# Kernel tuning notes

Measured on AMD Instinct MI355X. Metric: run time of the kernel, lower is better.

Reference implementation:

```python
import jax, jax.numpy as jnp
import numpy as np

N = 100000   # nodes
E = 1600000  # edges
F_IN = 4
H = 64
G = 1000     # graphs in batch
C = 3        # num_classes
L = 2        # num_unit (LEConv layers)


def setup_inputs() -> dict:
    key = jax.random.key(0)
    ks = jax.random.split(key, 14)
    s = 0.1
    return {
        "x": jax.random.normal(ks[0], (N, F_IN), jnp.float32),
        "edge_index": jax.random.randint(ks[1], (2, E), 0, N, dtype=jnp.int32),
        "edge_attr": jax.random.uniform(ks[2], (E,), jnp.float32),
        "batch": jnp.sort(jax.random.randint(ks[3], (N,), 0, G, dtype=jnp.int32)),
        "w_emb": jax.random.normal(ks[4], (F_IN, H), jnp.float32) * s,
        "b_emb": jnp.zeros((H,), jnp.float32),
        "lin1_w": jax.random.normal(ks[5], (L, H, H), jnp.float32) * s,
        "lin1_b": jnp.zeros((L, H), jnp.float32),
        "lin2_w": jax.random.normal(ks[6], (L, H, H), jnp.float32) * s,  # bias=False in PyG LEConv
        "lin3_w": jax.random.normal(ks[7], (L, H, H), jnp.float32) * s,
        "lin3_b": jnp.zeros((L, H), jnp.float32),
        "mlp_w1": jax.random.normal(ks[8], (H, 2 * H), jnp.float32) * s,
        "mlp_b1": jnp.zeros((2 * H,), jnp.float32),
        "mlp_w2": jax.random.normal(ks[9], (2 * H, C), jnp.float32) * s,
        "mlp_b2": jnp.zeros((C,), jnp.float32),
    }


def reference(x, edge_index, edge_attr, batch, w_emb, b_emb,
              lin1_w, lin1_b, lin2_w, lin3_w, lin3_b,
              mlp_w1, mlp_b1, mlp_w2, mlp_b2):
    src, dst = edge_index[0], edge_index[1]  # message flows src(j) -> dst(i)
    h = x @ w_emb + b_emb  # [N, H]
    for l in range(L):
        a = h @ lin1_w[l] + lin1_b[l]            # lin1(x_j) source side
        b = h @ lin2_w[l]                         # lin2(x_i) target side, no bias
        msg = (a[src] - b[dst]) * edge_attr[:, None]   # [E, H]
        agg = jax.ops.segment_sum(msg, dst, num_segments=N)
        h = jax.nn.relu(agg + h @ lin3_w[l] + lin3_b[l])
    # global_mean_pool
    sums = jax.ops.segment_sum(h, batch, num_segments=G)        # [G, H]
    counts = jax.ops.segment_sum(jnp.ones((N,), h.dtype), batch, num_segments=G)
    graph_x = sums / jnp.maximum(counts, 1.0)[:, None]
    # causal_mlp head
    return jax.nn.relu(graph_x @ mlp_w1 + mlp_b1) @ mlp_w2 + mlp_b2  # [G, C]
```

## Files before the change

### kernel.cpp

```cpp
#include <hip/hip_runtime.h>

#define N_NODES 100000
#define N_EDGES 1600000
#define F_INPUT 4
#define HDIM 64
#define G_GRAPHS 1000
#define C_CLS 3

#define NPB 256
#define BSHIFT 8
#define NB 391
#define CBLK 98
#define CSR_CAP 6144
#define HIST_BLOCKS 512
#define BNDS_BLOCKS 391

typedef __attribute__((ext_vector_type(8))) short bf16x8;
typedef __attribute__((ext_vector_type(4))) float f32x4;

__device__ __forceinline__ unsigned short f2bf(float f) {
    unsigned u = __float_as_uint(f);
    unsigned r = (u + 0x7FFF + ((u >> 16) & 1)) >> 16;
    return (unsigned short)r;
}
__device__ __forceinline__ float bflo(unsigned u) {
    return __uint_as_float(u << 16);
}
__device__ __forceinline__ float bfhi(unsigned u) {
    return __uint_as_float(u & 0xFFFF0000u);
}
__device__ __forceinline__ float bf1(unsigned short s) {
    return __uint_as_float(((unsigned)s) << 16);
}

__global__ __launch_bounds__(256) void k_prew(
    const float* __restrict__ w_emb, const float* __restrict__ b_emb,
    const float* __restrict__ lin1_w, const float* __restrict__ lin1_b,
    const float* __restrict__ lin2_w,
    const float* __restrict__ lin3_w, const float* __restrict__ lin3_b,
    float* __restrict__ wp, float* __restrict__ bp, int* __restrict__ bcnt) {
    int t = threadIdx.x;
    for (int i = t; i < NB; i += 256) bcnt[i] = 0;
    int k = t >> 6, f = t & 63;
    const float* Ws[3] = {lin1_w, lin2_w, lin3_w};
#pragma unroll
    for (int m = 0; m < 3; ++m) {
        float s = 0.f;
        for (int j = 0; j < HDIM; ++j) s += w_emb[k * HDIM + j] * Ws[m][j * HDIM + f];
        wp[m * 256 + k * HDIM + f] = s;
    }
    if (t < HDIM) {
#pragma unroll
        for (int m = 0; m < 3; ++m) {
            float s = 0.f;
            for (int j = 0; j < HDIM; ++j) s += b_emb[j] * Ws[m][j * HDIM + t];
            if (m == 0) s += lin1_b[t];
            if (m == 2) s += lin3_b[t];
            bp[m * HDIM + t] = s;
        }
    }
}

__global__ __launch_bounds__(256) void k_hist_bounds(
    const int* __restrict__ dst, int* __restrict__ bcnt,
    const int* __restrict__ batch, int* __restrict__ goff) {
    __shared__ int s[NB];
    if (blockIdx.x < HIST_BLOCKS) {
        int bb = blockIdx.x;
        for (int i = threadIdx.x; i < NB; i += 256) s[i] = 0;
        __syncthreads();
        for (int e = bb * 256 + threadIdx.x; e < N_EDGES; e += HIST_BLOCKS * 256)
            atomicAdd(&s[dst[e] >> BSHIFT], 1);
        __syncthreads();
        for (int i = threadIdx.x; i < NB; i += 256)
            if (s[i]) atomicAdd(&bcnt[i], s[i]);
    } else {
        int n = (blockIdx.x - HIST_BLOCKS) * 256 + threadIdx.x;
        if (n >= N_NODES) return;
        int bv = batch[n];
        int bp_ = (n == 0) ? -1 : batch[n - 1];
        for (int g = bp_ + 1; g <= bv; ++g) goff[g] = n;
        if (n == N_NODES - 1) {
            for (int g = bv + 1; g <= G_GRAPHS; ++g) goff[g] = N_NODES;
        }
    }
}

__global__ __launch_bounds__(512) void k_boff(
    const int* __restrict__ bcnt, int* __restrict__ boff, int* __restrict__ bcur) {
    __shared__ int s[512];
    int t = threadIdx.x;
    int v = (t < NB) ? bcnt[t] : 0;
    s[t] = v;
    __syncthreads();
    for (int d = 1; d < 512; d <<= 1) {
        int x2 = (t >= d) ? s[t - d] : 0;
        __syncthreads();
        s[t] += x2;
        __syncthreads();
    }
    int ex = s[t] - v;
    if (t < NB) { boff[t] = ex; bcur[t] = ex; }
    if (t == 0) boff[NB] = N_EDGES;
}

__global__ __launch_bounds__(1024) void k_bucket(const int* __restrict__ src,
                                                 const int* __restrict__ dst,
                                                 const float* __restrict__ attr,
                                                 int* __restrict__ bcur,
                                                 int2* __restrict__ bbuf) {
    __shared__ int cnt[NB];
    __shared__ int base[NB];
    for (int i = threadIdx.x; i < NB; i += 1024) cnt[i] = 0;
    __syncthreads();
    int e0 = blockIdx.x * 16384;
    int myb[16], myrank[16];
    int2 mypack[16];
#pragma unroll
    for (int k = 0; k < 16; ++k) {
        int e = e0 + k * 1024 + threadIdx.x;
        if (e < N_EDGES) {
            int d = dst[e];
            int b = d >> BSHIFT;
            myb[k] = b;
            myrank[k] = atomicAdd(&cnt[b], 1);
            mypack[k].x = src[e] | ((d & (NPB - 1)) << 17);
            mypack[k].y = __float_as_int(attr[e]);
        } else
            myb[k] = -1;
    }
    __syncthreads();
    for (int i = threadIdx.x; i < NB; i += 1024)
        base[i] = cnt[i] ? atomicAdd(&bcur[i], cnt[i]) : 0;
    __syncthreads();
#pragma unroll
    for (int k = 0; k < 16; ++k)
        if (myb[k] >= 0) bbuf[base[myb[k]] + myrank[k]] = mypack[k];
}

__global__ __launch_bounds__(256) void k_csr(const int2* __restrict__ bbuf,
                                             const int* __restrict__ boff,
                                             int* __restrict__ off,
                                             float* __restrict__ wsum,
                                             int2* __restrict__ edge2,
                                             const float* __restrict__ x,
                                             const float* __restrict__ wp,
                                             const float* __restrict__ bp,
                                             unsigned short* __restrict__ a_out,
                                             unsigned short* __restrict__ d_out_) {
    __shared__ int2 se[CSR_CAP];
    __shared__ int deg[NPB];
    __shared__ float wsm[NPB];
    __shared__ int loff[NPB];
    __shared__ int sct[256];
    int b = blockIdx.x;
    int lo = boff[b];
    int cnt = boff[b + 1] - lo;
    if (cnt > CSR_CAP) cnt = CSR_CAP;
    int t = threadIdx.x;
    deg[t] = 0;
    wsm[t] = 0.f;
    for (int i = t; i < cnt; i += 256) se[i] = bbuf[lo + i];
    __syncthreads();
    for (int i = t; i < cnt; i += 256) {
        int2 p = se[i];
        int dloc = (p.x >> 17) & (NPB - 1);
        atomicAdd(&deg[dloc], 1);
        atomicAdd(&wsm[dloc], __int_as_float(p.y));
    }
    __syncthreads();
    int v = deg[t];
    sct[t] = v;
    __syncthreads();
    for (int d = 1; d < 256; d <<= 1) {
        int x2 = (t >= d) ? sct[t - d] : 0;
        __syncthreads();
        sct[t] += x2;
        __syncthreads();
    }
    int ex = sct[t] - v;
    loff[t] = ex;
    __syncthreads();
    int n0 = b * NPB + t;
    if (n0 < N_NODES) { off[n0] = lo + ex; wsum[n0] = wsm[t]; }
    if (b == NB - 1 && t == 0) off[N_NODES] = N_EDGES;
    deg[t] = 0;
    __syncthreads();
    for (int i = t; i < cnt; i += 256) {
        int2 p = se[i];
        int dloc = (p.x >> 17) & (NPB - 1);
        int r = atomicAdd(&deg[dloc], 1);
        edge2[lo + loff[dloc] + r] = make_int2(p.x & 0x1FFFF, p.y);
    }

    {
        int wave = t >> 6, lane = t & 63;
        int row = lane & 15, kg = lane >> 4;
        int col = wave * 16 + row;
        bf16x8 Bf[3];
#pragma unroll
        for (int m = 0; m < 3; ++m) {
            union { bf16x8 v; unsigned short u[8]; } fr;
#pragma unroll
            for (int j = 0; j < 8; ++j)
                fr.u[j] = (kg == 0 && j < F_INPUT) ? f2bf(wp[m * 256 + j * HDIM + col])
                                                   : (unsigned short)0;
            Bf[m] = fr.v;
        }
        float bias1 = bp[col], bias2 = bp[HDIM + col], bias3 = bp[2 * HDIM + col];
        int base = b * NPB;
        for (int tt = 0; tt < 16; ++tt) {
            int n = base + tt * 16 + row;
            union { bf16x8 v; unsigned short u[8]; } af;
#pragma unroll
            for (int j = 0; j < 8; ++j) af.u[j] = 0;
            if (kg == 0 && n < N_NODES) {
                float4 xv = *(const float4*)(x + (size_t)n * F_INPUT);
                af.u[0] = f2bf(xv.x); af.u[1] = f2bf(xv.y);
                af.u[2] = f2bf(xv.z); af.u[3] = f2bf(xv.w);
            }
            f32x4 ac0 = (f32x4){0.f, 0.f, 0.f, 0.f};
            f32x4 ac1 = (f32x4){0.f, 0.f, 0.f, 0.f};
            f32x4 ac2 = (f32x4){0.f, 0.f, 0.f, 0.f};
            ac0 = __builtin_amdgcn_mfma_f32_16x16x32_bf16(af.v, Bf[0], ac0, 0, 0, 0);
            ac1 = __builtin_amdgcn_mfma_f32_16x16x32_bf16(af.v, Bf[1], ac1, 0, 0, 0);
            ac2 = __builtin_amdgcn_mfma_f32_16x16x32_bf16(af.v, Bf[2], ac2, 0, 0, 0);
#pragma unroll
            for (int r = 0; r < 4; ++r) {
                int nn = base + tt * 16 + kg * 4 + r;
                if (nn >= N_NODES) continue;
                float ws = wsm[tt * 16 + kg * 4 + r];
                float av = ac0[r] + bias1;
                float dv = ac2[r] + bias3 - (ac1[r] + bias2) * ws;
                a_out[(size_t)nn * HDIM + col] = f2bf(av);
                d_out_[(size_t)nn * HDIM + col] = f2bf(dv);
            }
        }
    }
}

__global__ __launch_bounds__(256) void k_gemm3(
    const unsigned short* __restrict__ h,
    const float* __restrict__ W1, const float* __restrict__ b1,
    const float* __restrict__ W2,
    const float* __restrict__ W3, const float* __restrict__ b3,
    const float* __restrict__ wsum,
    unsigned short* __restrict__ a_out, unsigned short* __restrict__ d_out_) {
    int wave = threadIdx.x >> 6;
    int lane = threadIdx.x & 63;
    int row = lane & 15;
    int kg = lane >> 4;
    int base = blockIdx.x * 64;
    int col = wave * 16 + row;

    bf16x8 Bf[3][2];
    const float* Ws[3] = {W1, W2, W3};
#pragma unroll
    for (int m = 0; m < 3; ++m)
#pragma unroll
        for (int hf = 0; hf < 2; ++hf) {
            union { bf16x8 v; unsigned short u[8]; } fr;
#pragma unroll
            for (int j = 0; j < 8; ++j) {
                int k = hf * 32 + kg * 8 + j;
                fr.u[j] = f2bf(Ws[m][k * HDIM + col]);
            }
            Bf[m][hf] = fr.v;
        }

    float bias1 = b1[col];
    float bias3 = b3[col];

    f32x4 acc[3][4];
#pragma unroll
    for (int m = 0; m < 3; ++m)
#pragma unroll
        for (int t = 0; t < 4; ++t) acc[m][t] = (f32x4){0.f, 0.f, 0.f, 0.f};

#pragma unroll
    for (int t = 0; t < 4; ++t) {
        int n = base + t * 16 + row;
        bf16x8 a0, a1;
        if (n < N_NODES) {
            const unsigned short* hr = h + (size_t)n * HDIM;
            a0 = *(const bf16x8*)(hr + kg * 8);
            a1 = *(const bf16x8*)(hr + 32 + kg * 8);
        } else {
            a0 = (bf16x8){0,0,0,0,0,0,0,0};
            a1 = (bf16x8){0,0,0,0,0,0,0,0};
        }
#pragma unroll
        for (int m = 0; m < 3; ++m) {
            acc[m][t] = __builtin_amdgcn_mfma_f32_16x16x32_bf16(a0, Bf[m][0], acc[m][t], 0, 0, 0);
            acc[m][t] = __builtin_amdgcn_mfma_f32_16x16x32_bf16(a1, Bf[m][1], acc[m][t], 0, 0, 0);
        }
    }

#pragma unroll
    for (int t = 0; t < 4; ++t) {
#pragma unroll
        for (int r = 0; r < 4; ++r) {
            int n = base + t * 16 + kg * 4 + r;
            if (n >= N_NODES) continue;
            float ws = wsum[n];
            float av = acc[0][t][r] + bias1;
            float dv = acc[2][t][r] + bias3 - acc[1][t][r] * ws;
            a_out[(size_t)n * HDIM + col] = f2bf(av);
            d_out_[(size_t)n * HDIM + col] = f2bf(dv);
        }
    }
}

__global__ __launch_bounds__(256) void k_agg(const int2* __restrict__ edge2,
                                             const int* __restrict__ off,
                                             const unsigned short* __restrict__ a,
                                             const unsigned short* __restrict__ dbuf,
                                             unsigned short* __restrict__ h) {
    int wid = threadIdx.x >> 6;
    int lane = threadIdx.x & 63;
    int slot = lane >> 3;
    int fo = lane & 7;
    int n = blockIdx.x * 4 + wid;
    if (n >= N_NODES) return;
    int lo = off[n], hi = off[n + 1];

    float acc[8];
#pragma unroll
    for (int q = 0; q < 8; ++q) acc[q] = 0.f;

#define GATHER_ADD(J)                                                        \
    if ((J) < hi) {                                                          \
        int2 p = edge2[(J)];                                                 \
        float w = __int_as_float(p.y);                                       \
        uint4 u = *(const uint4*)(a + (size_t)p.x * HDIM + fo * 8);          \
        acc[0] += bflo(u.x) * w; acc[1] += bfhi(u.x) * w;                    \
        acc[2] += bflo(u.y) * w; acc[3] += bfhi(u.y) * w;                    \
        acc[4] += bflo(u.z) * w; acc[5] += bfhi(u.z) * w;                    \
        acc[6] += bflo(u.w) * w; acc[7] += bfhi(u.w) * w;                    \
    }

    for (int j0 = lo; j0 < hi; j0 += 32) {
        GATHER_ADD(j0 + slot)
        GATHER_ADD(j0 + 8 + slot)
        GATHER_ADD(j0 + 16 + slot)
        GATHER_ADD(j0 + 24 + slot)
    }
#undef GATHER_ADD

#pragma unroll
    for (int m = 8; m <= 32; m <<= 1) {
#pragma unroll
        for (int q = 0; q < 8; ++q) acc[q] += __shfl_xor(acc[q], m);
    }

    if (slot == 0) {
        size_t o = (size_t)n * HDIM + fo * 8;
        uint4 dv = *(const uint4*)(dbuf + o);
        float dd[8] = {bflo(dv.x), bfhi(dv.x), bflo(dv.y), bfhi(dv.y),
                       bflo(dv.z), bfhi(dv.z), bflo(dv.w), bfhi(dv.w)};
        unsigned r[4];
#pragma unroll
        for (int q = 0; q < 4; ++q) {
            unsigned lo16 = f2bf(fmaxf(acc[2 * q] + dd[2 * q], 0.f));
            unsigned hi16 = f2bf(fmaxf(acc[2 * q + 1] + dd[2 * q + 1], 0.f));
            r[q] = lo16 | (hi16 << 16);
        }
        *(uint4*)(h + o) = make_uint4(r[0], r[1], r[2], r[3]);
    }
}

__global__ __launch_bounds__(256) void k_poolhead(const unsigned short* __restrict__ h,
                                                  const int* __restrict__ goff,
                                                  const float* __restrict__ W1,
                                                  const float* __restrict__ b1,
                                                  const float* __restrict__ W2,
                                                  const float* __restrict__ b2,
                                                  float* __restrict__ out) {
    int g = blockIdx.x;
    __shared__ float part[256];
    __shared__ float sx[HDIM];
    __shared__ float sy[2 * HDIM];
    int t = threadIdx.x;
    int lo = goff[g], hi = goff[g + 1];
    int f = t & 63, quarter = t >> 6;
    float acc = 0.f;
    for (int n = lo + quarter; n < hi; n += 4) acc += bf1(h[(size_t)n * HDIM + f]);
    part[t] = acc;
    __syncthreads();
    if (t < HDIM)
        sx[t] = (part[t] + part[t + 64] + part[t + 128] + part[t + 192]) /
                fmaxf((float)(hi - lo), 1.f);
    __syncthreads();
    if (t < 2 * HDIM) {
        float a1 = b1[t];
        for (int k = 0; k < HDIM; ++k) a1 += sx[k] * W1[k * 2 * HDIM + t];
        sy[t] = fmaxf(a1, 0.f);
    }
    __syncthreads();
    if (t < C_CLS) {
        float o = b2[t];
        for (int k = 0; k < 2 * HDIM; ++k) o += sy[k] * W2[k * C_CLS + t];
        out[g * C_CLS + t] = o;
    }
}

extern "C" void kernel_launch(void* const* d_in, const int* in_sizes, int n_in,
                              void* d_out, int out_size, void* d_ws, size_t ws_size,
                              hipStream_t stream) {
    const float* x      = (const float*)d_in[0];
    const int*   ei     = (const int*)d_in[1];
    const float* eattr  = (const float*)d_in[2];
    const int*   batch  = (const int*)d_in[3];
    const float* w_emb  = (const float*)d_in[4];
    const float* b_emb  = (const float*)d_in[5];
    const float* lin1_w = (const float*)d_in[6];
    const float* lin1_b = (const float*)d_in[7];
    const float* lin2_w = (const float*)d_in[8];
    const float* lin3_w = (const float*)d_in[9];
    const float* lin3_b = (const float*)d_in[10];
    const float* mlp_w1 = (const float*)d_in[11];
    const float* mlp_b1 = (const float*)d_in[12];
    const float* mlp_w2 = (const float*)d_in[13];
    const float* mlp_b2 = (const float*)d_in[14];
    float* out = (float*)d_out;

    const int* src = ei;
    const int* dst = ei + N_EDGES;

    const size_t NH = (size_t)N_NODES * HDIM;
    unsigned short* abf = (unsigned short*)d_ws;
    unsigned short* dbf = abf + NH;
    unsigned short* h   = dbf + NH;
    float* wsum = (float*)(h + NH);
    int2* edge2 = (int2*)(wsum + N_NODES);
    int2* bbuf  = edge2 + N_EDGES;
    int* off    = (int*)(bbuf + N_EDGES);
    int* bcnt   = off + N_NODES + 1;
    int* bcur   = bcnt + NB;
    int* boff   = bcur + NB;
    int* goff   = boff + NB + 1;
    float* wp   = (float*)(goff + G_GRAPHS + 1);
    float* bp   = wp + 3 * 256;

    k_prew<<<1, 256, 0, stream>>>(w_emb, b_emb,
                                  lin1_w, lin1_b, lin2_w, lin3_w, lin3_b, wp, bp, bcnt);
    k_hist_bounds<<<HIST_BLOCKS + BNDS_BLOCKS, 256, 0, stream>>>(dst, bcnt, batch, goff);
    k_boff<<<1, 512, 0, stream>>>(bcnt, boff, bcur);
    k_bucket<<<CBLK, 1024, 0, stream>>>(src, dst, eattr, bcur, bbuf);
    k_csr<<<NB, 256, 0, stream>>>(bbuf, boff, off, wsum, edge2, x, wp, bp, abf, dbf);

    int gemm_blocks = (N_NODES + 63) / 64;
    int agg_blocks = (N_NODES + 3) / 4;

    k_agg<<<agg_blocks, 256, 0, stream>>>(edge2, off, abf, dbf, h);
    k_gemm3<<<gemm_blocks, 256, 0, stream>>>(h, lin1_w + HDIM * HDIM, lin1_b + HDIM,
                                             lin2_w + HDIM * HDIM,
                                             lin3_w + HDIM * HDIM, lin3_b + HDIM,
                                             wsum, abf, dbf);
    k_agg<<<agg_blocks, 256, 0, stream>>>(edge2, off, abf, dbf, h);
    k_poolhead<<<G_GRAPHS, 256, 0, stream>>>(h, goff, mlp_w1, mlp_b1, mlp_w2, mlp_b2, out);
}
```

Baseline: 234.9 us.

## Split first-layer GEMM out of CSR kernel and vectorize histogram loads

Moves the first-layer embedding GEMM, which computes a and d, out of the 391-block CSR kernel into a separate kernel launched with one block per 64 nodes. The first layer therefore runs across many more blocks instead of serially looping 16 tiles inside each CSR block. The edge histogram now reads dst as int4, four edges per load. The split adds a kernel launch and a global reread of wsum, where the old code read it from shared memory.

```diff
diff --git a/kernel.cpp b/kernel.cpp
--- a/kernel.cpp
+++ b/kernel.cpp
@@ -69,8 +69,14 @@
         int bb = blockIdx.x;
         for (int i = threadIdx.x; i < NB; i += 256) s[i] = 0;
         __syncthreads();
-        for (int e = bb * 256 + threadIdx.x; e < N_EDGES; e += HIST_BLOCKS * 256)
-            atomicAdd(&s[dst[e] >> BSHIFT], 1);
+        const int4* dst4 = (const int4*)dst;
+        for (int e4 = bb * 256 + threadIdx.x; e4 < N_EDGES / 4; e4 += HIST_BLOCKS * 256) {
+            int4 d = dst4[e4];
+            atomicAdd(&s[d.x >> BSHIFT], 1);
+            atomicAdd(&s[d.y >> BSHIFT], 1);
+            atomicAdd(&s[d.z >> BSHIFT], 1);
+            atomicAdd(&s[d.w >> BSHIFT], 1);
+        }
         __syncthreads();
         for (int i = threadIdx.x; i < NB; i += 256)
             if (s[i]) atomicAdd(&bcnt[i], s[i]);
@@ -142,12 +148,7 @@
                                              const int* __restrict__ boff,
                                              int* __restrict__ off,
                                              float* __restrict__ wsum,
-                                             int2* __restrict__ edge2,
-                                             const float* __restrict__ x,
-                                             const float* __restrict__ wp,
-                                             const float* __restrict__ bp,
-                                             unsigned short* __restrict__ a_out,
-                                             unsigned short* __restrict__ d_out_) {
+                                             int2* __restrict__ edge2) {
     __shared__ int2 se[CSR_CAP];
     __shared__ int deg[NPB];
     __shared__ float wsm[NPB];
@@ -181,8 +182,8 @@
     int ex = sct[t] - v;
     loff[t] = ex;
     __syncthreads();
-    int n0 = b * NPB + t;
-    if (n0 < N_NODES) { off[n0] = lo + ex; wsum[n0] = wsm[t]; }
+    int n = b * NPB + t;
+    if (n < N_NODES) { off[n] = lo + ex; wsum[n] = wsm[t]; }
     if (b == NB - 1 && t == 0) off[N_NODES] = N_EDGES;
     deg[t] = 0;
     __syncthreads();
@@ -192,49 +193,64 @@
         int r = atomicAdd(&deg[dloc], 1);
         edge2[lo + loff[dloc] + r] = make_int2(p.x & 0x1FFFF, p.y);
     }
-
-    {
-        int wave = t >> 6, lane = t & 63;
-        int row = lane & 15, kg = lane >> 4;
-        int col = wave * 16 + row;
-        bf16x8 Bf[3];
-#pragma unroll
-        for (int m = 0; m < 3; ++m) {
-            union { bf16x8 v; unsigned short u[8]; } fr;
-#pragma unroll
-            for (int j = 0; j < 8; ++j)
-                fr.u[j] = (kg == 0 && j < F_INPUT) ? f2bf(wp[m * 256 + j * HDIM + col])
-                                                   : (unsigned short)0;
-            Bf[m] = fr.v;
-        }
-        float bias1 = bp[col], bias2 = bp[HDIM + col], bias3 = bp[2 * HDIM + col];
-        int base = b * NPB;
-        for (int tt = 0; tt < 16; ++tt) {
-            int n = base + tt * 16 + row;
-            union { bf16x8 v; unsigned short u[8]; } af;
-#pragma unroll
-            for (int j = 0; j < 8; ++j) af.u[j] = 0;
-            if (kg == 0 && n < N_NODES) {
-                float4 xv = *(const float4*)(x + (size_t)n * F_INPUT);
-                af.u[0] = f2bf(xv.x); af.u[1] = f2bf(xv.y);
-                af.u[2] = f2bf(xv.z); af.u[3] = f2bf(xv.w);
-            }
-            f32x4 ac0 = (f32x4){0.f, 0.f, 0.f, 0.f};
-            f32x4 ac1 = (f32x4){0.f, 0.f, 0.f, 0.f};
-            f32x4 ac2 = (f32x4){0.f, 0.f, 0.f, 0.f};
-            ac0 = __builtin_amdgcn_mfma_f32_16x16x32_bf16(af.v, Bf[0], ac0, 0, 0, 0);
-            ac1 = __builtin_amdgcn_mfma_f32_16x16x32_bf16(af.v, Bf[1], ac1, 0, 0, 0);
-            ac2 = __builtin_amdgcn_mfma_f32_16x16x32_bf16(af.v, Bf[2], ac2, 0, 0, 0);
-#pragma unroll
-            for (int r = 0; r < 4; ++r) {
-                int nn = base + tt * 16 + kg * 4 + r;
-                if (nn >= N_NODES) continue;
-                float ws = wsm[tt * 16 + kg * 4 + r];
-                float av = ac0[r] + bias1;
-                float dv = ac2[r] + bias3 - (ac1[r] + bias2) * ws;
-                a_out[(size_t)nn * HDIM + col] = f2bf(av);
-                d_out_[(size_t)nn * HDIM + col] = f2bf(dv);
-            }
+}
+
+__global__ __launch_bounds__(256) void k_gemm1st(
+    const float* __restrict__ x, const float* __restrict__ wp,
+    const float* __restrict__ bp, const float* __restrict__ wsum,
+    unsigned short* __restrict__ a_out, unsigned short* __restrict__ d_out_) {
+    int wave = threadIdx.x >> 6;
+    int lane = threadIdx.x & 63;
+    int row = lane & 15;
+    int kg = lane >> 4;
+    int base = blockIdx.x * 64;
+    int col = wave * 16 + row;
+
+    bf16x8 Bf[3];
+#pragma unroll
+    for (int m = 0; m < 3; ++m) {
+        union { bf16x8 v; unsigned short u[8]; } fr;
+#pragma unroll
+        for (int j = 0; j < 8; ++j)
+            fr.u[j] = (kg == 0 && j < F_INPUT) ? f2bf(wp[m * 256 + j * HDIM + col])
+                                               : (unsigned short)0;
+        Bf[m] = fr.v;
+    }
+    float bias1 = bp[col], bias2 = bp[HDIM + col], bias3 = bp[2 * HDIM + col];
+
+    f32x4 acc[3][4];
+#pragma unroll
+    for (int m = 0; m < 3; ++m)
+#pragma unroll
+        for (int t = 0; t < 4; ++t) acc[m][t] = (f32x4){0.f, 0.f, 0.f, 0.f};
+
+#pragma unroll
+    for (int t = 0; t < 4; ++t) {
+        int n = base + t * 16 + row;
+        union { bf16x8 v; unsigned short u[8]; } af;
+#pragma unroll
+        for (int j = 0; j < 8; ++j) af.u[j] = 0;
+        if (kg == 0 && n < N_NODES) {
+            float4 xv = *(const float4*)(x + (size_t)n * F_INPUT);
+            af.u[0] = f2bf(xv.x); af.u[1] = f2bf(xv.y);
+            af.u[2] = f2bf(xv.z); af.u[3] = f2bf(xv.w);
+        }
+#pragma unroll
+        for (int m = 0; m < 3; ++m)
+            acc[m][t] = __builtin_amdgcn_mfma_f32_16x16x32_bf16(af.v, Bf[m], acc[m][t], 0, 0, 0);
+    }
+
+#pragma unroll
+    for (int t = 0; t < 4; ++t) {
+#pragma unroll
+        for (int r = 0; r < 4; ++r) {
+            int n = base + t * 16 + kg * 4 + r;
+            if (n >= N_NODES) continue;
+            float ws = wsum[n];
+            float av = acc[0][t][r] + bias1;
+            float dv = acc[2][t][r] + bias3 - (acc[1][t][r] + bias2) * ws;
+            a_out[(size_t)n * HDIM + col] = f2bf(av);
+            d_out_[(size_t)n * HDIM + col] = f2bf(dv);
         }
     }
 }
@@ -447,11 +463,12 @@
     k_hist_bounds<<<HIST_BLOCKS + BNDS_BLOCKS, 256, 0, stream>>>(dst, bcnt, batch, goff);
     k_boff<<<1, 512, 0, stream>>>(bcnt, boff, bcur);
     k_bucket<<<CBLK, 1024, 0, stream>>>(src, dst, eattr, bcur, bbuf);
-    k_csr<<<NB, 256, 0, stream>>>(bbuf, boff, off, wsum, edge2, x, wp, bp, abf, dbf);
+    k_csr<<<NB, 256, 0, stream>>>(bbuf, boff, off, wsum, edge2);
 
     int gemm_blocks = (N_NODES + 63) / 64;
     int agg_blocks = (N_NODES + 3) / 4;
 
+    k_gemm1st<<<gemm_blocks, 256, 0, stream>>>(x, wp, bp, wsum, abf, dbf);
     k_agg<<<agg_blocks, 256, 0, stream>>>(edge2, off, abf, dbf, h);
     k_gemm3<<<gemm_blocks, 256, 0, stream>>>(h, lin1_w + HDIM * HDIM, lin1_b + HDIM,
                                              lin2_w + HDIM * HDIM,
```

Result: faster. 228.2 us (median of 2 runs) (-2.9%).
